# Kernel optimization log

Measured on AMD Instinct MI355X. Metric: run time of the kernel, lower is better.

The kernel has to match this reference:

```python
import math
import jax, jax.numpy as jnp
import numpy as np

B, S, IN_DIM = 4, 2048, 256
L, H, NHEAD, FFN = 3, 256, 4, 1024
CF, CB = 32, 32  # context_forward / context_backward window
EPS = 1e-5


def sinusoidal_pe(seq_len, d_model):
    pos = jnp.arange(seq_len, dtype=jnp.float32)[:, None]
    div = jnp.exp(jnp.arange(0, d_model, 2, dtype=jnp.float32) * (-math.log(10000.0) / d_model))
    pe = jnp.zeros((seq_len, d_model), dtype=jnp.float32)
    pe = pe.at[:, 0::2].set(jnp.sin(pos * div))
    pe = pe.at[:, 1::2].set(jnp.cos(pos * div))
    return pe


def band_mask(s):
    # True = allowed: -CB <= j - i <= CF (sliding window, from triu/transpose construction)
    i = jnp.arange(s)[:, None]
    j = jnp.arange(s)[None, :]
    return (j - i <= CF) & (i - j <= CB)


def layer_norm(x, g, b):
    mu = jnp.mean(x, axis=-1, keepdims=True)
    var = jnp.mean((x - mu) ** 2, axis=-1, keepdims=True)
    return (x - mu) * jax.lax.rsqrt(var + EPS) * g + b


def mha(x, wqkv, bqkv, wo, bo, mask):
    b, s, d = x.shape
    dh = d // NHEAD
    qkv = x @ wqkv.T + bqkv  # [b, s, 3d]
    q, k, v = jnp.split(qkv, 3, axis=-1)
    split = lambda t: t.reshape(b, s, NHEAD, dh).transpose(0, 2, 1, 3)  # [b, h, s, dh]
    q, k, v = split(q), split(k), split(v)
    scores = jnp.einsum('bhqd,bhkd->bhqk', q, k) / math.sqrt(dh)
    scores = jnp.where(mask, scores, -jnp.inf)
    attn = jax.nn.softmax(scores, axis=-1)
    o = jnp.einsum('bhqk,bhkd->bhqd', attn, v).transpose(0, 2, 1, 3).reshape(b, s, d)
    return o @ wo.T + bo


def setup_inputs() -> dict:
    key = jax.random.key(0)
    ks = jax.random.split(key, 12)
    sc = 0.02
    inp = {
        'x': jax.random.normal(ks[0], (B, S, IN_DIM), dtype=jnp.float32),
        'w_in': sc * jax.random.normal(ks[1], (H, IN_DIM), dtype=jnp.float32),
        'w_out': sc * jax.random.normal(ks[2], (IN_DIM, H), dtype=jnp.float32),
        'b_out': jnp.zeros((IN_DIM,), dtype=jnp.float32),
        'qkv_w': sc * jax.random.normal(ks[3], (L, 3 * H, H), dtype=jnp.float32),
        'qkv_b': jnp.zeros((L, 3 * H), dtype=jnp.float32),
        'out_w': sc * jax.random.normal(ks[4], (L, H, H), dtype=jnp.float32),
        'out_b': jnp.zeros((L, H), dtype=jnp.float32),
        'ln1_g': jnp.ones((L, H), dtype=jnp.float32),
        'ln1_b': jnp.zeros((L, H), dtype=jnp.float32),
        'ln2_g': jnp.ones((L, H), dtype=jnp.float32),
        'ln2_b': jnp.zeros((L, H), dtype=jnp.float32),
        'ff1_w': sc * jax.random.normal(ks[5], (L, FFN, H), dtype=jnp.float32),
        'ff1_b': jnp.zeros((L, FFN), dtype=jnp.float32),
        'ff2_w': sc * jax.random.normal(ks[6], (L, H, FFN), dtype=jnp.float32),
        'ff2_b': jnp.zeros((L, H), dtype=jnp.float32),
        'lnf_g': jnp.ones((H,), dtype=jnp.float32),
        'lnf_b': jnp.zeros((H,), dtype=jnp.float32),
    }
    return inp


def reference(x, w_in, w_out, b_out, qkv_w, qkv_b, out_w, out_b,
              ln1_g, ln1_b, ln2_g, ln2_b, ff1_w, ff1_b, ff2_w, ff2_b,
              lnf_g, lnf_b):
    b, s, _ = x.shape
    mask = band_mask(s)
    h = math.sqrt(H) * (x @ w_in.T) + sinusoidal_pe(s, H)[None]
    for l in range(L):  # pre-norm transformer encoder layers (relu FFN, eval/no-dropout)
        h = h + mha(layer_norm(h, ln1_g[l], ln1_b[l]), qkv_w[l], qkv_b[l], out_w[l], out_b[l], mask)
        z = layer_norm(h, ln2_g[l], ln2_b[l])
        h = h + (jax.nn.relu(z @ ff1_w[l].T + ff1_b[l]) @ ff2_w[l].T + ff2_b[l])
    h = layer_norm(h, lnf_g, lnf_b)
    return h @ w_out.T + b_out
```

## Files before the change

### kernel.cpp

```cpp
#include <hip/hip_runtime.h>
#include <hip/hip_bf16.h>
#include <math.h>

#define SEQ 2048
#define BATCH 4
#define HDIM 256
#define NHEAD 4
#define FFN_DIM 1024
#define MTOT (BATCH*SEQ)

typedef __attribute__((ext_vector_type(8))) short bf16x8;
typedef __attribute__((ext_vector_type(4))) float f32x4;

__device__ __forceinline__ bf16x8 cvt8(const float* p)
{
    float4 a = *(const float4*)p;
    float4 b = *(const float4*)(p + 4);
    union { bf16x8 v; __hip_bfloat16 e[8]; } u;
    u.e[0] = __float2bfloat16(a.x); u.e[1] = __float2bfloat16(a.y);
    u.e[2] = __float2bfloat16(a.z); u.e[3] = __float2bfloat16(a.w);
    u.e[4] = __float2bfloat16(b.x); u.e[5] = __float2bfloat16(b.y);
    u.e[6] = __float2bfloat16(b.z); u.e[7] = __float2bfloat16(b.w);
    return u.v;
}

__global__ __launch_bounds__(256)
void cvt_all(const float* __restrict__ w_in, const float* __restrict__ w_out,
             const float* __restrict__ qkv_w, const float* __restrict__ out_w,
             const float* __restrict__ ff1_w, const float* __restrict__ ff2_w,
             __hip_bfloat16* __restrict__ wb)
{
    int i = blockIdx.x * 256 + threadIdx.x;
    size_t e = (size_t)i * 8;

    const float* srcbase; size_t rbase; int kshift;
    if (e < 720896) {
        if (e < 65536)       { srcbase = w_in;  rbase = 0;      kshift = 8; }
        else if (e < 131072) { srcbase = w_out; rbase = 65536;  kshift = 8; }
        else                 { srcbase = qkv_w; rbase = 131072; kshift = 8; }
    } else if (e < 917504)   { srcbase = out_w; rbase = 720896; kshift = 8; }
    else if (e < 1703936)    { srcbase = ff1_w; rbase = 917504; kshift = 8; }
    else                     { srcbase = ff2_w; rbase = 1703936; kshift = 10; }

    size_t local = e - rbase;
    int K = 1 << kshift;
    int row = (int)(local >> kshift);
    int k   = (int)(local & (K - 1));

    size_t dst = rbase
               + ((size_t)(row >> 4) * (K >> 5) + (k >> 5)) * 512
               + (size_t)((((k >> 3) & 3) << 4) | (row & 15)) * 8;

    *(bf16x8*)(wb + dst) = cvt8(srcbase + local);
}

__device__ __forceinline__ bf16x8 fragW(const short* W, int n0, int k0, int K, int lane)
{
    return *(const bf16x8*)(W + ((size_t)(n0 >> 4) * (K >> 5) + (k0 >> 5)) * 512 + lane * 8);
}

__device__ __forceinline__ size_t qkv_idx(int row, int col)
{
    int sec = col >> 8, hd = (col >> 6) & 3, d = col & 63;
    int srow = row & (SEQ - 1);
    size_t base = (size_t)sec * 2097152
                + (size_t)(((row >> 11) << 2) | hd) * 131072;
    if (sec < 2)
        return base + (size_t)(srow >> 4) * 1024 + (size_t)(d >> 5) * 512
             + (size_t)((((d >> 3) & 3) << 4) | (srow & 15)) * 8 + (d & 7);
    return base + (size_t)srow * 64 + d;
}

__device__ __forceinline__ void ln_rows(const float (*H)[260], short (*A)[264],
                                        const float* __restrict__ g,
                                        const float* __restrict__ bl,
                                        int wave, int lane)
{
    float4 gv = *(const float4*)(g + lane * 4);
    float4 bv = *(const float4*)(bl + lane * 4);
    #pragma unroll
    for (int u = 0; u < 2; u++) {
        float4 xv = *(const float4*)&H[wave*2 + u][lane*4];
        float ss2 = xv.x + xv.y + xv.z + xv.w;
        #pragma unroll
        for (int off = 32; off >= 1; off >>= 1) ss2 += __shfl_xor(ss2, off);
        float mu = ss2 * (1.0f/256.0f);
        float d0 = xv.x-mu, d1 = xv.y-mu, d2 = xv.z-mu, d3 = xv.w-mu;
        float v = d0*d0 + d1*d1 + d2*d2 + d3*d3;
        #pragma unroll
        for (int off = 32; off >= 1; off >>= 1) v += __shfl_xor(v, off);
        float rstd = rsqrtf(v * (1.0f/256.0f) + 1e-5f);
        union { short e[4]; uint2 w2; } o;
        o.e[0] = (short)__bfloat16_as_ushort(__float2bfloat16(d0*rstd*gv.x + bv.x));
        o.e[1] = (short)__bfloat16_as_ushort(__float2bfloat16(d1*rstd*gv.y + bv.y));
        o.e[2] = (short)__bfloat16_as_ushort(__float2bfloat16(d2*rstd*gv.z + bv.z));
        o.e[3] = (short)__bfloat16_as_ushort(__float2bfloat16(d3*rstd*gv.w + bv.w));
        *(uint2*)&A[wave*2 + u][lane*4] = o.w2;
    }
}

__global__ __launch_bounds__(1024)
void embed_qkv(const float* __restrict__ X,
               const __hip_bfloat16* __restrict__ wb,
               const float* __restrict__ ln1_g, const float* __restrict__ ln1_b,
               const float* __restrict__ qkv_b,
               float* __restrict__ h, __hip_bfloat16* __restrict__ qkvd)
{
    __shared__ __align__(16) float H_lds[32][260];
    __shared__ __align__(16) short A_lds[32][264];

    int tid = threadIdx.x, wave = tid >> 6, lane = tid & 63;
    int b = blockIdx.y, i0 = blockIdx.x * 32;
    int lr = lane & 15, hi = lane >> 4;
    int cc = lane & 15, quad = lane >> 4;
    const short* wbs = (const short*)wb;

    {
        const float* px0 = X + (size_t)(b*SEQ + i0 + lr) * HDIM + hi * 8;
        const float* px1 = px0 + (size_t)16 * HDIM;
        f32x4 acc[2];
        acc[0] = (f32x4){0.f,0.f,0.f,0.f}; acc[1] = (f32x4){0.f,0.f,0.f,0.f};
        #pragma unroll
        for (int k0 = 0; k0 < 256; k0 += 32) {
            bf16x8 a0 = cvt8(px0 + k0);
            bf16x8 a1 = cvt8(px1 + k0);
            bf16x8 b0 = fragW(wbs, wave*16, k0, 256, lane);
            acc[0] = __builtin_amdgcn_mfma_f32_16x16x32_bf16(a0, b0, acc[0], 0,0,0);
            acc[1] = __builtin_amdgcn_mfma_f32_16x16x32_bf16(a1, b0, acc[1], 0,0,0);
        }
        int col = wave*16 + cc;
        int i2 = col & ~1;
        float freq = __expf((float)i2 * (-9.210340371976184f / 256.0f));
        #pragma unroll
        for (int mt = 0; mt < 2; mt++)
            #pragma unroll
            for (int r = 0; r < 4; r++) {
                int rowl = mt*16 + quad*4 + r;
                int srow = i0 + rowl;
                float arg = (float)srow * freq;
                float pe = (col & 1) ? __cosf(arg) : __sinf(arg);
                float v = 16.0f*acc[mt][r] + pe;
                H_lds[rowl][col] = v;
                h[(size_t)(b*SEQ + srow) * HDIM + col] = v;
            }
    }
    __syncthreads();

    ln_rows(H_lds, A_lds, ln1_g, ln1_b, wave, lane);
    __syncthreads();

    {
        const short* Wts = wbs + 131072;
        f32x4 qa[2][3];
        #pragma unroll
        for (int mt = 0; mt < 2; mt++)
            #pragma unroll
            for (int nt = 0; nt < 3; nt++)
                qa[mt][nt] = (f32x4){0.f,0.f,0.f,0.f};
        #pragma unroll
        for (int k0 = 0; k0 < 256; k0 += 32) {
            bf16x8 a0 = *(const bf16x8*)&A_lds[lr][k0 + hi*8];
            bf16x8 a1 = *(const bf16x8*)&A_lds[16 + lr][k0 + hi*8];
            #pragma unroll
            for (int nt = 0; nt < 3; nt++) {
                bf16x8 wf = fragW(Wts, wave*48 + nt*16, k0, 256, lane);
                qa[0][nt] = __builtin_amdgcn_mfma_f32_16x16x32_bf16(a0, wf, qa[0][nt], 0,0,0);
                qa[1][nt] = __builtin_amdgcn_mfma_f32_16x16x32_bf16(a1, wf, qa[1][nt], 0,0,0);
            }
        }
        #pragma unroll
        for (int nt = 0; nt < 3; nt++) {
            int col = wave*48 + nt*16 + cc;
            float bv = qkv_b[col];
            #pragma unroll
            for (int mt = 0; mt < 2; mt++)
                #pragma unroll
                for (int r = 0; r < 4; r++) {
                    int row = b * SEQ + i0 + mt*16 + quad*4 + r;
                    qkvd[qkv_idx(row, col)] = __float2bfloat16(qa[mt][nt][r] + bv);
                }
        }
    }
}

struct AttnLDS {
    __align__(16) __hip_bfloat16 Vt[64][128];
    __align__(16) __hip_bfloat16 Pl[32][96];
    float sm[2][32], ss[2][32];
};

template<int TAIL>
__global__ __launch_bounds__(1024)
void attn_ffn(const __hip_bfloat16* __restrict__ qkvd,
              const __hip_bfloat16* __restrict__ ow,
              const float* __restrict__ ob,
              float* __restrict__ h,
              const float* __restrict__ g, const float* __restrict__ bln,
              const __hip_bfloat16* __restrict__ W1, const float* __restrict__ b1,
              const __hip_bfloat16* __restrict__ W2, const float* __restrict__ b2,
              const float* __restrict__ gt, const float* __restrict__ bt,
              const __hip_bfloat16* __restrict__ Wt, const float* __restrict__ btb,
              float* __restrict__ outp, __hip_bfloat16* __restrict__ qkv_out)
{
    __shared__ union SMem {
        AttnLDS asl[4];
        struct {
            __align__(16) short A[32][264];
            __align__(16) short Z[2][32][264];
        } f;
    } U;
    __shared__ __align__(16) short att_lds[32][264];
    __shared__ __align__(16) float H_lds[32][260];

    int tid  = threadIdx.x;
    int wave = tid >> 6, lane = tid & 63;
    int grp  = wave >> 2, w4 = wave & 3, ltid = tid & 255;
    int b    = blockIdx.y, i0 = blockIdx.x * 32;
    int klo  = i0 - 32;

    int lr = lane & 15, hi = lane >> 4;
    int cc = lane & 15, quad = lane >> 4;

    int hd = grp;
    AttnLDS& S = U.asl[grp];
    const short* Qd = (const short*)qkvd + (size_t)(b * 4 + hd) * 131072;
    const short* Kd = Qd + 2097152;
    const short* Vd = Qd + 4194304;
    int qh = w4 & 1, seg = w4 >> 1;
    int qoff = qh * 16 + quad * 4;

    int vm = ltid & 7, vrl = ltid >> 3, vdp = vm * 8;
    bf16x8 vr[3];
    #pragma unroll
    for (int rr = 0; rr < 3; rr++) {
        int j = klo + rr * 32 + vrl;
        j = j < 0 ? 0 : (j > SEQ - 1 ? SEQ - 1 : j);
        vr[rr] = *(const bf16x8*)(Vd + (size_t)j * 64 + vdp);
    }
    bf16x8 qf[2];
    #pragma unroll
    for (int ds = 0; ds < 2; ds++)
        qf[ds] = *(const bf16x8*)(Qd + (size_t)((i0 >> 4) + qh) * 1024 + ds * 512 + lane * 8);
    bf16x8 kf[3][2];
    #pragma unroll
    for (int t = 0; t < 3; t++) {
        int jt = (klo + seg * 48 + t * 16) >> 4;
        jt = jt < 0 ? 0 : (jt > 127 ? 127 : jt);
        kf[t][0] = *(const bf16x8*)(Kd + (size_t)jt * 1024 + lane * 8);
        kf[t][1] = *(const bf16x8*)(Kd + (size_t)jt * 1024 + 512 + lane * 8);
    }
    float hold[2][4];
    {
        const float* hp = h + (size_t)(b * SEQ + i0) * HDIM + wave * 16 + cc;
        #pragma unroll
        for (int mt = 0; mt < 2; mt++)
            #pragma unroll
            for (int r = 0; r < 4; r++)
                hold[mt][r] = hp[(size_t)(mt*16 + quad*4 + r) * HDIM];
    }

    {
        union { bf16x8 v; short e[8]; } u;
        #pragma unroll
        for (int rr = 0; rr < 3; rr++) {
            int row = rr * 32 + vrl;
            int colp = row ^ (vm << 3);
            u.v = vr[rr];
            #pragma unroll
            for (int jj = 0; jj < 8; jj++)
                *(short*)&S.Vt[vdp + jj][colp] = u.e[jj];
        }
    }

    f32x4 sacc[3];
    #pragma unroll
    for (int t = 0; t < 3; t++) {
        f32x4 a = (f32x4){0.f,0.f,0.f,0.f};
        a = __builtin_amdgcn_mfma_f32_16x16x32_bf16(qf[0], kf[t][0], a, 0,0,0);
        a = __builtin_amdgcn_mfma_f32_16x16x32_bf16(qf[1], kf[t][1], a, 0,0,0);
        sacc[t] = a;
    }

    float s[3][4];
    #pragma unroll
    for (int t = 0; t < 3; t++) {
        int koff = seg * 48 + t * 16 + cc;
        int jj = klo + koff;
        #pragma unroll
        for (int r = 0; r < 4; r++) {
            int rel = koff - (qoff + r);
            bool ok = (jj >= 0) && (jj < SEQ) && (rel >= 0) && (rel <= 64);
            s[t][r] = ok ? sacc[t][r] * 0.125f : -1e30f;
        }
    }

    float mrow[4], srow[4];
    #pragma unroll
    for (int r = 0; r < 4; r++)
        mrow[r] = fmaxf(fmaxf(s[0][r], s[1][r]), s[2][r]);
    #pragma unroll
    for (int off = 8; off >= 1; off >>= 1)
        #pragma unroll
        for (int r = 0; r < 4; r++)
            mrow[r] = fmaxf(mrow[r], __shfl_xor(mrow[r], off));
    #pragma unroll
    for (int r = 0; r < 4; r++)
        srow[r] = __expf(s[0][r]-mrow[r]) + __expf(s[1][r]-mrow[r]) + __expf(s[2][r]-mrow[r]);
    #pragma unroll
    for (int off = 8; off >= 1; off >>= 1)
        #pragma unroll
        for (int r = 0; r < 4; r++)
            srow[r] += __shfl_xor(srow[r], off);
    if (cc == 0) {
        #pragma unroll
        for (int r = 0; r < 4; r++) { S.sm[seg][qoff+r] = mrow[r]; S.ss[seg][qoff+r] = srow[r]; }
    }
    __syncthreads();

    float Mr[4], inv[4];
    #pragma unroll
    for (int r = 0; r < 4; r++) {
        float m0 = S.sm[0][qoff+r], m1 = S.sm[1][qoff+r];
        float M = fmaxf(m0, m1);
        float dn = S.ss[0][qoff+r] * __expf(m0 - M) + S.ss[1][qoff+r] * __expf(m1 - M);
        Mr[r] = M; inv[r] = 1.0f / dn;
    }
    #pragma unroll
    for (int t = 0; t < 3; t++)
        #pragma unroll
        for (int r = 0; r < 4; r++)
            S.Pl[qoff+r][seg*48 + t*16 + cc] = __float2bfloat16(__expf(s[t][r]-Mr[r]) * inv[r]);
    __syncthreads();

    bf16x8 owf[8];
    {
        const short* op = (const short*)ow + (size_t)wave * 8 * 512 + lane * 8;
        #pragma unroll
        for (int i = 0; i < 8; i++)
            owf[i] = *(const bf16x8*)(op + i * 512);
    }

    {
        f32x4 oacc[2];
        oacc[0] = (f32x4){0.f,0.f,0.f,0.f}; oacc[1] = (f32x4){0.f,0.f,0.f,0.f};
        #pragma unroll
        for (int ks = 0; ks < 3; ks++) {
            int kk = ks * 32;
            bf16x8 pf = *(const bf16x8*)&S.Pl[qh*16 + lr][kk + hi*8];
            #pragma unroll
            for (int dt = 0; dt < 2; dt++) {
                int d = seg*32 + dt*16 + lr;
                int colb = (kk + hi*8) ^ (((d >> 3) & 7) << 3);
                bf16x8 vf = *(const bf16x8*)&S.Vt[d][colb];
                oacc[dt] = __builtin_amdgcn_mfma_f32_16x16x32_bf16(pf, vf, oacc[dt], 0,0,0);
            }
        }
        #pragma unroll
        for (int dt = 0; dt < 2; dt++) {
            int col = hd*64 + seg*32 + dt*16 + cc;
            #pragma unroll
            for (int r = 0; r < 4; r++)
                att_lds[qoff + r][col] =
                    (short)__bfloat16_as_ushort(__float2bfloat16(oacc[dt][r]));
        }
    }
    __syncthreads();

    {
        f32x4 acc[2];
        acc[0] = (f32x4){0.f,0.f,0.f,0.f}; acc[1] = (f32x4){0.f,0.f,0.f,0.f};
        #pragma unroll
        for (int i = 0; i < 8; i++) {
            bf16x8 a0 = *(const bf16x8*)&att_lds[lr][i*32 + hi*8];
            bf16x8 a1 = *(const bf16x8*)&att_lds[16 + lr][i*32 + hi*8];
            acc[0] = __builtin_amdgcn_mfma_f32_16x16x32_bf16(a0, owf[i], acc[0], 0,0,0);
            acc[1] = __builtin_amdgcn_mfma_f32_16x16x32_bf16(a1, owf[i], acc[1], 0,0,0);
        }
        float bv = ob[wave*16 + cc];
        #pragma unroll
        for (int mt = 0; mt < 2; mt++)
            #pragma unroll
            for (int r = 0; r < 4; r++)
                H_lds[mt*16 + quad*4 + r][wave*16 + cc] = hold[mt][r] + acc[mt][r] + bv;
    }

    const short* W1s = (const short*)W1;
    const short* W2s = (const short*)W2;
    bf16x8 w1f[8];
    {
        const short* wp = W1s + (size_t)wave * 8 * 512 + lane * 8;
        #pragma unroll
        for (int i = 0; i < 8; i++)
            w1f[i] = *(const bf16x8*)(wp + i * 512);
    }
    __syncthreads();

    ln_rows(H_lds, U.f.A, g, bln, wave, lane);
    __syncthreads();

    f32x4 acc2[2];
    acc2[0] = (f32x4){0.f,0.f,0.f,0.f}; acc2[1] = (f32x4){0.f,0.f,0.f,0.f};

    #pragma unroll 1
    for (int kk = 0; kk < 4; kk++) {
        bf16x8 w2f[8];
        {
            const short* wp = W2s + (size_t)(wave * 32 + kk * 8) * 512 + lane * 8;
            #pragma unroll
            for (int i = 0; i < 8; i++)
                w2f[i] = *(const bf16x8*)(wp + i * 512);
        }

        f32x4 acc1[2];
        acc1[0] = (f32x4){0.f,0.f,0.f,0.f}; acc1[1] = (f32x4){0.f,0.f,0.f,0.f};
        #pragma unroll
        for (int i = 0; i < 8; i++) {
            bf16x8 af0 = *(const bf16x8*)&U.f.A[lr][i*32 + hi*8];
            bf16x8 af1 = *(const bf16x8*)&U.f.A[16 + lr][i*32 + hi*8];
            acc1[0] = __builtin_amdgcn_mfma_f32_16x16x32_bf16(af0, w1f[i], acc1[0], 0,0,0);
            acc1[1] = __builtin_amdgcn_mfma_f32_16x16x32_bf16(af1, w1f[i], acc1[1], 0,0,0);
        }

        {
            int col = wave*16 + cc;
            float bb = b1[kk*256 + col];
            #pragma unroll
            for (int mt = 0; mt < 2; mt++)
                #pragma unroll
                for (int r = 0; r < 4; r++) {
                    float z = fmaxf(acc1[mt][r] + bb, 0.f);
                    U.f.Z[kk & 1][mt*16 + quad*4 + r][col] =
                        (short)__bfloat16_as_ushort(__float2bfloat16(z));
                }
        }
        __syncthreads();

        {
            int nk = (kk < 3) ? kk + 1 : 3;
            const short* wp = W1s + (size_t)(nk * 16 + wave) * 8 * 512 + lane * 8;
            #pragma unroll
            for (int i = 0; i < 8; i++)
                w1f[i] = *(const bf16x8*)(wp + i * 512);
        }

        #pragma unroll
        for (int i = 0; i < 8; i++) {
            bf16x8 zf0 = *(const bf16x8*)&U.f.Z[kk & 1][lr][i*32 + hi*8];
            bf16x8 zf1 = *(const bf16x8*)&U.f.Z[kk & 1][16 + lr][i*32 + hi*8];
            acc2[0] = __builtin_amdgcn_mfma_f32_16x16x32_bf16(zf0, w2f[i], acc2[0], 0,0,0);
            acc2[1] = __builtin_amdgcn_mfma_f32_16x16x32_bf16(zf1, w2f[i], acc2[1], 0,0,0);
        }
    }

    {
        int col = wave*16 + cc;
        float bb = b2[col];
        #pragma unroll
        for (int mt = 0; mt < 2; mt++)
            #pragma unroll
            for (int r = 0; r < 4; r++) {
                int rowl = mt*16 + quad*4 + r;
                float v = H_lds[rowl][col] + acc2[mt][r] + bb;
                H_lds[rowl][col] = v;
                if (TAIL == 1) {
                    int row = b * SEQ + i0 + rowl;
                    h[(size_t)row * HDIM + col] = v;
                }
            }
    }
    __syncthreads();

    ln_rows(H_lds, U.f.A, gt, bt, wave, lane);
    __syncthreads();

    if (TAIL == 2) {
        bf16x8 wf[8];
        const short* wp = (const short*)Wt + (size_t)wave * 8 * 512 + lane * 8;
        #pragma unroll
        for (int i = 0; i < 8; i++)
            wf[i] = *(const bf16x8*)(wp + i * 512);

        f32x4 oa[2];
        oa[0] = (f32x4){0.f,0.f,0.f,0.f}; oa[1] = (f32x4){0.f,0.f,0.f,0.f};
        #pragma unroll
        for (int i = 0; i < 8; i++) {
            bf16x8 a0 = *(const bf16x8*)&U.f.A[lr][i*32 + hi*8];
            bf16x8 a1 = *(const bf16x8*)&U.f.A[16 + lr][i*32 + hi*8];
            oa[0] = __builtin_amdgcn_mfma_f32_16x16x32_bf16(a0, wf[i], oa[0], 0,0,0);
            oa[1] = __builtin_amdgcn_mfma_f32_16x16x32_bf16(a1, wf[i], oa[1], 0,0,0);
        }
        int col = wave*16 + cc;
        float bb = btb[col];
        #pragma unroll
        for (int mt = 0; mt < 2; mt++)
            #pragma unroll
            for (int r = 0; r < 4; r++) {
                int row = b * SEQ + i0 + mt*16 + quad*4 + r;
                outp[(size_t)row * HDIM + col] = oa[mt][r] + bb;
            }
    } else {
        const short* Wts = (const short*)Wt;
        f32x4 qa[2][3];
        #pragma unroll
        for (int mt = 0; mt < 2; mt++)
            #pragma unroll
            for (int nt = 0; nt < 3; nt++)
                qa[mt][nt] = (f32x4){0.f,0.f,0.f,0.f};

        #pragma unroll
        for (int k0 = 0; k0 < 256; k0 += 32) {
            bf16x8 a0 = *(const bf16x8*)&U.f.A[lr][k0 + hi*8];
            bf16x8 a1 = *(const bf16x8*)&U.f.A[16 + lr][k0 + hi*8];
            #pragma unroll
            for (int nt = 0; nt < 3; nt++) {
                bf16x8 wf = fragW(Wts, wave*48 + nt*16, k0, 256, lane);
                qa[0][nt] = __builtin_amdgcn_mfma_f32_16x16x32_bf16(a0, wf, qa[0][nt], 0,0,0);
                qa[1][nt] = __builtin_amdgcn_mfma_f32_16x16x32_bf16(a1, wf, qa[1][nt], 0,0,0);
            }
        }
        #pragma unroll
        for (int nt = 0; nt < 3; nt++) {
            int col = wave*48 + nt*16 + cc;
            float bv = btb[col];
            #pragma unroll
            for (int mt = 0; mt < 2; mt++)
                #pragma unroll
                for (int r = 0; r < 4; r++) {
                    int row = b * SEQ + i0 + mt*16 + quad*4 + r;
                    qkv_out[qkv_idx(row, col)] = __float2bfloat16(qa[mt][nt][r] + bv);
                }
        }
    }
}

extern "C" void kernel_launch(void* const* d_in, const int* in_sizes, int n_in,
                              void* d_out, int out_size, void* d_ws, size_t ws_size,
                              hipStream_t stream)
{
    const float* x     = (const float*)d_in[0];
    const float* w_in  = (const float*)d_in[1];
    const float* w_out = (const float*)d_in[2];
    const float* b_out = (const float*)d_in[3];
    const float* qkv_w = (const float*)d_in[4];
    const float* qkv_b = (const float*)d_in[5];
    const float* out_w = (const float*)d_in[6];
    const float* out_b = (const float*)d_in[7];
    const float* ln1_g = (const float*)d_in[8];
    const float* ln1_b = (const float*)d_in[9];
    const float* ln2_g = (const float*)d_in[10];
    const float* ln2_b = (const float*)d_in[11];
    const float* ff1_w = (const float*)d_in[12];
    const float* ff1_b = (const float*)d_in[13];
    const float* ff2_w = (const float*)d_in[14];
    const float* ff2_b = (const float*)d_in[15];
    const float* lnf_g = (const float*)d_in[16];
    const float* lnf_b = (const float*)d_in[17];

    char* ws = (char*)d_ws;
    float*          h     = (float*)ws;
    __hip_bfloat16* qkvd0 = (__hip_bfloat16*)(ws + 8388608);
    __hip_bfloat16* qkvd1 = (__hip_bfloat16*)(ws + 20971520);
    __hip_bfloat16* wb    = (__hip_bfloat16*)(ws + 33554432);

    __hip_bfloat16* w_out_b = wb + 65536;
    __hip_bfloat16* qkv_w_b = wb + 131072;
    __hip_bfloat16* out_w_b = wb + 720896;
    __hip_bfloat16* ff1_w_b = wb + 917504;
    __hip_bfloat16* ff2_w_b = wb + 1703936;

    cvt_all<<<1216, dim3(256), 0, stream>>>(w_in, w_out, qkv_w, out_w, ff1_w, ff2_w, wb);

    embed_qkv<<<dim3(SEQ/32, BATCH), dim3(1024), 0, stream>>>(
        x, wb, ln1_g, ln1_b, qkv_b, h, qkvd0);

    attn_ffn<1><<<dim3(SEQ/32, BATCH), dim3(1024), 0, stream>>>(
        qkvd0, out_w_b, out_b, h,
        ln2_g, ln2_b, ff1_w_b, ff1_b, ff2_w_b, ff2_b,
        ln1_g + HDIM, ln1_b + HDIM,
        qkv_w_b + (size_t)768*HDIM, qkv_b + 768, nullptr, qkvd1);

    attn_ffn<1><<<dim3(SEQ/32, BATCH), dim3(1024), 0, stream>>>(
        qkvd1, out_w_b + (size_t)HDIM*HDIM, out_b + HDIM, h,
        ln2_g + HDIM, ln2_b + HDIM,
        ff1_w_b + (size_t)FFN_DIM*HDIM, ff1_b + FFN_DIM,
        ff2_w_b + (size_t)HDIM*FFN_DIM, ff2_b + HDIM,
        ln1_g + 2*HDIM, ln1_b + 2*HDIM,
        qkv_w_b + (size_t)2*768*HDIM, qkv_b + 2*768, nullptr, qkvd0);

    attn_ffn<2><<<dim3(SEQ/32, BATCH), dim3(1024), 0, stream>>>(
        qkvd0, out_w_b + (size_t)2*HDIM*HDIM, out_b + 2*HDIM, h,
        ln2_g + 2*HDIM, ln2_b + 2*HDIM,
        ff1_w_b + (size_t)2*FFN_DIM*HDIM, ff1_b + 2*FFN_DIM,
        ff2_w_b + (size_t)2*HDIM*FFN_DIM, ff2_b + 2*HDIM,
        lnf_g, lnf_b, w_out_b, b_out, (float*)d_out, nullptr);
}
```

Baseline: 220.9 us.

## Store V in MFMA-fragment layout and load directly to registers, shrink LDS

The QKV projection now writes V already tiled in the B-operand fragment layout the MFMA expects. The attention kernel can therefore load V fragments straight from global memory into registers, with no transpose through LDS. This removes the scalar LDS transpose stores and the swizzled reads, and frees the Vt buffer. The LDS union is reorganised and the Z double buffer becomes a single buffer with an extra barrier, which lowers LDS footprint but adds one sync per FFN chunk.

```diff
diff --git a/kernel.cpp b/kernel.cpp
--- a/kernel.cpp
+++ b/kernel.cpp
@@ -68,7 +68,8 @@
     if (sec < 2)
         return base + (size_t)(srow >> 4) * 1024 + (size_t)(d >> 5) * 512
              + (size_t)((((d >> 3) & 3) << 4) | (srow & 15)) * 8 + (d & 7);
-    return base + (size_t)srow * 64 + d;
+    return base + ((size_t)(d >> 4) * 64 + (srow >> 5)) * 512
+         + (size_t)((((srow >> 3) & 3) << 4) | (d & 15)) * 8 + (srow & 7);
 }
 
 __device__ __forceinline__ void ln_rows(const float (*H)[260], short (*A)[264],
@@ -183,8 +184,7 @@
     }
 }
 
-struct AttnLDS {
-    __align__(16) __hip_bfloat16 Vt[64][128];
+struct AttnSm {
     __align__(16) __hip_bfloat16 Pl[32][96];
     float sm[2][32], ss[2][32];
 };
@@ -203,18 +203,14 @@
               float* __restrict__ outp, __hip_bfloat16* __restrict__ qkv_out)
 {
     __shared__ union SMem {
-        AttnLDS asl[4];
-        struct {
-            __align__(16) short A[32][264];
-            __align__(16) short Z[2][32][264];
-        } f;
+        struct { AttnSm asl[4]; __align__(16) short att[32][264]; } a;
+        struct { __align__(16) short A[32][264]; __align__(16) short Z[32][264]; } f;
     } U;
-    __shared__ __align__(16) short att_lds[32][264];
     __shared__ __align__(16) float H_lds[32][260];
 
     int tid  = threadIdx.x;
     int wave = tid >> 6, lane = tid & 63;
-    int grp  = wave >> 2, w4 = wave & 3, ltid = tid & 255;
+    int grp  = wave >> 2, w4 = wave & 3;
     int b    = blockIdx.y, i0 = blockIdx.x * 32;
     int klo  = i0 - 32;
 
@@ -222,21 +218,13 @@
     int cc = lane & 15, quad = lane >> 4;
 
     int hd = grp;
-    AttnLDS& S = U.asl[grp];
+    AttnSm& S = U.a.asl[grp];
     const short* Qd = (const short*)qkvd + (size_t)(b * 4 + hd) * 131072;
     const short* Kd = Qd + 2097152;
     const short* Vd = Qd + 4194304;
     int qh = w4 & 1, seg = w4 >> 1;
     int qoff = qh * 16 + quad * 4;
 
-    int vm = ltid & 7, vrl = ltid >> 3, vdp = vm * 8;
-    bf16x8 vr[3];
-    #pragma unroll
-    for (int rr = 0; rr < 3; rr++) {
-        int j = klo + rr * 32 + vrl;
-        j = j < 0 ? 0 : (j > SEQ - 1 ? SEQ - 1 : j);
-        vr[rr] = *(const bf16x8*)(Vd + (size_t)j * 64 + vdp);
-    }
     bf16x8 qf[2];
     #pragma unroll
     for (int ds = 0; ds < 2; ds++)
@@ -249,6 +237,17 @@
         kf[t][0] = *(const bf16x8*)(Kd + (size_t)jt * 1024 + lane * 8);
         kf[t][1] = *(const bf16x8*)(Kd + (size_t)jt * 1024 + 512 + lane * 8);
     }
+    bf16x8 vf[3][2];
+    #pragma unroll
+    for (int ks = 0; ks < 3; ks++) {
+        int s0 = klo + ks * 32;
+        s0 = s0 < 0 ? 0 : (s0 > SEQ - 32 ? SEQ - 32 : s0);
+        #pragma unroll
+        for (int dt = 0; dt < 2; dt++) {
+            int d0 = seg*32 + dt*16;
+            vf[ks][dt] = *(const bf16x8*)(Vd + ((size_t)(d0 >> 4) * 64 + (s0 >> 5)) * 512 + lane * 8);
+        }
+    }
     float hold[2][4];
     {
         const float* hp = h + (size_t)(b * SEQ + i0) * HDIM + wave * 16 + cc;
@@ -257,19 +256,6 @@
             #pragma unroll
             for (int r = 0; r < 4; r++)
                 hold[mt][r] = hp[(size_t)(mt*16 + quad*4 + r) * HDIM];
-    }
-
-    {
-        union { bf16x8 v; short e[8]; } u;
-        #pragma unroll
-        for (int rr = 0; rr < 3; rr++) {
-            int row = rr * 32 + vrl;
-            int colp = row ^ (vm << 3);
-            u.v = vr[rr];
-            #pragma unroll
-            for (int jj = 0; jj < 8; jj++)
-                *(short*)&S.Vt[vdp + jj][colp] = u.e[jj];
-        }
     }
 
     f32x4 sacc[3];
@@ -345,22 +331,17 @@
         oacc[0] = (f32x4){0.f,0.f,0.f,0.f}; oacc[1] = (f32x4){0.f,0.f,0.f,0.f};
         #pragma unroll
         for (int ks = 0; ks < 3; ks++) {
-            int kk = ks * 32;
-            bf16x8 pf = *(const bf16x8*)&S.Pl[qh*16 + lr][kk + hi*8];
-            #pragma unroll
-            for (int dt = 0; dt < 2; dt++) {
-                int d = seg*32 + dt*16 + lr;
-                int colb = (kk + hi*8) ^ (((d >> 3) & 7) << 3);
-                bf16x8 vf = *(const bf16x8*)&S.Vt[d][colb];
-                oacc[dt] = __builtin_amdgcn_mfma_f32_16x16x32_bf16(pf, vf, oacc[dt], 0,0,0);
-            }
+            bf16x8 pf = *(const bf16x8*)&S.Pl[qh*16 + lr][ks*32 + hi*8];
+            #pragma unroll
+            for (int dt = 0; dt < 2; dt++)
+                oacc[dt] = __builtin_amdgcn_mfma_f32_16x16x32_bf16(pf, vf[ks][dt], oacc[dt], 0,0,0);
         }
         #pragma unroll
         for (int dt = 0; dt < 2; dt++) {
             int col = hd*64 + seg*32 + dt*16 + cc;
             #pragma unroll
             for (int r = 0; r < 4; r++)
-                att_lds[qoff + r][col] =
+                U.a.att[qoff + r][col] =
                     (short)__bfloat16_as_ushort(__float2bfloat16(oacc[dt][r]));
         }
     }
@@ -371,8 +352,8 @@
         acc[0] = (f32x4){0.f,0.f,0.f,0.f}; acc[1] = (f32x4){0.f,0.f,0.f,0.f};
         #pragma unroll
         for (int i = 0; i < 8; i++) {
-            bf16x8 a0 = *(const bf16x8*)&att_lds[lr][i*32 + hi*8];
-            bf16x8 a1 = *(const bf16x8*)&att_lds[16 + lr][i*32 + hi*8];
+            bf16x8 a0 = *(const bf16x8*)&U.a.att[lr][i*32 + hi*8];
+            bf16x8 a1 = *(const bf16x8*)&U.a.att[16 + lr][i*32 + hi*8];
             acc[0] = __builtin_amdgcn_mfma_f32_16x16x32_bf16(a0, owf[i], acc[0], 0,0,0);
             acc[1] = __builtin_amdgcn_mfma_f32_16x16x32_bf16(a1, owf[i], acc[1], 0,0,0);
         }
@@ -429,7 +410,7 @@
                 #pragma unroll
                 for (int r = 0; r < 4; r++) {
                     float z = fmaxf(acc1[mt][r] + bb, 0.f);
-                    U.f.Z[kk & 1][mt*16 + quad*4 + r][col] =
+                    U.f.Z[mt*16 + quad*4 + r][col] =
                         (short)__bfloat16_as_ushort(__float2bfloat16(z));
                 }
         }
@@ -445,11 +426,12 @@
 
         #pragma unroll
         for (int i = 0; i < 8; i++) {
-            bf16x8 zf0 = *(const bf16x8*)&U.f.Z[kk & 1][lr][i*32 + hi*8];
-            bf16x8 zf1 = *(const bf16x8*)&U.f.Z[kk & 1][16 + lr][i*32 + hi*8];
+            bf16x8 zf0 = *(const bf16x8*)&U.f.Z[lr][i*32 + hi*8];
+            bf16x8 zf1 = *(const bf16x8*)&U.f.Z[16 + lr][i*32 + hi*8];
             acc2[0] = __builtin_amdgcn_mfma_f32_16x16x32_bf16(zf0, w2f[i], acc2[0], 0,0,0);
             acc2[1] = __builtin_amdgcn_mfma_f32_16x16x32_bf16(zf1, w2f[i], acc2[1], 0,0,0);
         }
+        __syncthreads();
     }
 
     {
```

New measurement: 221.2 us. No clear change (+0.1%).
